# Performance work log

Measured on AMD Instinct MI355X. Metric: run time of the kernel, lower is better.

## Reference

```python
import jax, jax.numpy as jnp
import numpy as np

B, LQ, LK = 4, 256, 512
DQ = DK = PROJ = 256


def setup_inputs() -> dict:
    key = jax.random.key(0)
    ks = jax.random.split(key, 8)
    query = jax.random.normal(ks[0], (B, LQ, DQ), dtype=jnp.float32)
    keys = jax.random.normal(ks[1], (B, LK, DK), dtype=jnp.float32)
    attn_mask = jax.random.bernoulli(ks[2], 0.1, (B, LQ, LK))
    # Linear(query_size+key_size, proj) split into query/key halves (same math as concat @ W1)
    s1 = 1.0 / np.sqrt(DQ + DK)
    Wq = jax.random.uniform(ks[3], (DQ, PROJ), jnp.float32, -s1, s1)
    Wk = jax.random.uniform(ks[4], (DK, PROJ), jnp.float32, -s1, s1)
    b1 = jax.random.uniform(ks[5], (PROJ,), jnp.float32, -s1, s1)
    s2 = 1.0 / np.sqrt(PROJ)
    w2 = jax.random.uniform(ks[6], (PROJ,), jnp.float32, -s2, s2)
    b2 = jax.random.uniform(ks[7], (), jnp.float32, -s2, s2)
    return {"query": query, "keys": keys, "attn_mask": attn_mask,
            "Wq": Wq, "Wk": Wk, "b1": b1, "w2": w2, "b2": b2}


def reference(query, keys, attn_mask, Wq, Wk, b1, w2, b2):
    # cat(q_expand, k_expand) @ W1 == q@Wq broadcast-added to k@Wk (avoids the huge concat)
    qp = jnp.einsum('bqd,dp->bqp', query, Wq)            # (B,Lq,P)
    kp = jnp.einsum('bkd,dp->bkp', keys, Wk)             # (B,Lk,P)
    h = jnp.tanh(qp[:, :, None, :] + kp[:, None, :, :] + b1)  # (B,Lq,Lk,P)
    logits = jnp.einsum('bqkp,p->bqk', h, w2) + b2        # (B,Lq,Lk)
    logits = jnp.where(attn_mask, -jnp.inf, logits)
    return logits
```

## Files before the change

kernel.cpp:

```cpp
#include <hip/hip_runtime.h>
#include <math.h>

#define B_ 4
#define LQ_ 256
#define LK_ 512
#define D_ 256
#define P_ 256

#define SC 2.8853900817779268f

#define MASK_SENTINEL (-3.0e38f)


__global__ __launch_bounds__(256) void proj_kernel(
    const float* __restrict__ Q, const float* __restrict__ Kx,
    const float* __restrict__ Wq, const float* __restrict__ Wk,
    const float* __restrict__ b1,
    float* __restrict__ Eq, float* __restrict__ Ek)
{
    __shared__ __align__(16) float Ws[256][68];

    const int bm = blockIdx.x;
    const int bn = blockIdx.y;
    const bool isq = (bm < 32);
    const int m0 = isq ? bm * 32 : (bm - 32) * 32;
    const float* A = isq ? Q : Kx;
    const float* W = isq ? Wq : Wk;
    float* outp    = isq ? Eq : Ek;
    const int n0 = bn * 64;

    const int t  = threadIdx.x;
    const int tx = t & 15;
    const int ty = t >> 4;

    #pragma unroll
    for (int i = 0; i < 16; ++i) {
        int f  = t + i * 256;
        int r  = f >> 4;
        int c4 = (f & 15) * 4;
        *(float4*)&Ws[r][c4] = *(const float4*)&W[(size_t)r * P_ + n0 + c4];
    }
    __syncthreads();

    const float* arow0 = A + (size_t)(m0 + ty) * D_;
    const float* arow1 = A + (size_t)(m0 + ty + 16) * D_;

    float acc[2][4] = {};

    float4 a0c = *(const float4*)&arow0[0];
    float4 a1c = *(const float4*)&arow1[0];
    float4 w0c = *(const float4*)&Ws[0][tx * 4];
    float4 w1c = *(const float4*)&Ws[1][tx * 4];
    float4 w2c = *(const float4*)&Ws[2][tx * 4];
    float4 w3c = *(const float4*)&Ws[3][tx * 4];

    #pragma unroll 4
    for (int k4 = 0; k4 < 64; ++k4) {
        float4 a0 = a0c, a1 = a1c, w0 = w0c, w1 = w1c, w2v = w2c, w3 = w3c;
        if (k4 < 63) {
            a0c = *(const float4*)&arow0[(k4 + 1) * 4];
            a1c = *(const float4*)&arow1[(k4 + 1) * 4];
            w0c = *(const float4*)&Ws[k4 * 4 + 4][tx * 4];
            w1c = *(const float4*)&Ws[k4 * 4 + 5][tx * 4];
            w2c = *(const float4*)&Ws[k4 * 4 + 6][tx * 4];
            w3c = *(const float4*)&Ws[k4 * 4 + 7][tx * 4];
        }
        float av[2][4] = {{a0.x,a0.y,a0.z,a0.w},{a1.x,a1.y,a1.z,a1.w}};
        float wv[4][4] = {{w0.x,w0.y,w0.z,w0.w},{w1.x,w1.y,w1.z,w1.w},
                          {w2v.x,w2v.y,w2v.z,w2v.w},{w3.x,w3.y,w3.z,w3.w}};
        #pragma unroll
        for (int kk = 0; kk < 4; ++kk)
            #pragma unroll
            for (int i = 0; i < 2; ++i)
                #pragma unroll
                for (int j = 0; j < 4; ++j)
                    acc[i][j] = fmaf(av[i][kk], wv[kk][j], acc[i][j]);
    }

    float bv[4] = {0.f, 0.f, 0.f, 0.f};
    if (!isq) {
        float4 b = *(const float4*)&b1[n0 + tx * 4];
        bv[0] = b.x; bv[1] = b.y; bv[2] = b.z; bv[3] = b.w;
    }

    #pragma unroll
    for (int i = 0; i < 2; ++i) {
        int m = m0 + ty + i * 16;
        float4 o;
        o.x = __builtin_amdgcn_exp2f(SC * (acc[i][0] + bv[0]));
        o.y = __builtin_amdgcn_exp2f(SC * (acc[i][1] + bv[1]));
        o.z = __builtin_amdgcn_exp2f(SC * (acc[i][2] + bv[2]));
        o.w = __builtin_amdgcn_exp2f(SC * (acc[i][3] + bv[3]));
        *(float4*)&outp[(size_t)m * P_ + n0 + tx * 4] = o;
    }
}

__global__ __launch_bounds__(256, 4) void logits_kernel(
    const float* __restrict__ Eq, const float* __restrict__ Ek,
    const unsigned char* __restrict__ mask,
    const float* __restrict__ w2, const float* __restrict__ b2,
    float* __restrict__ out)
{
    __shared__ __align__(16) float eqs[32][132];
    __shared__ __align__(16) float eks[32][132];
    __shared__ float partial[4];

    const int b  = blockIdx.z;
    const int q0 = blockIdx.y * 32;
    const int k0 = blockIdx.x * 32;
    const int t  = threadIdx.x;

    const int tx = t & 15;
    const int ty = t >> 4;

    size_t oidx[2][2];
    unsigned char mb[2][2];
    #pragma unroll
    for (int i = 0; i < 2; ++i)
        #pragma unroll
        for (int j = 0; j < 2; ++j) {
            oidx[i][j] = (size_t)(b * LQ_ + q0 + ty + i * 16) * LK_ + (k0 + tx + j * 16);
            mb[i][j] = mask[oidx[i][j]];
        }

    float wv = w2[t];
    #pragma unroll
    for (int s = 32; s > 0; s >>= 1) wv += __shfl_xor(wv, s);
    if ((t & 63) == 0) partial[t >> 6] = wv;

    float acc[2][2] = {};

    for (int pc = 0; pc < 2; ++pc) {
        __syncthreads();
        const int p0 = pc * 128;
        #pragma unroll
        for (int i = 0; i < 2; ++i) {
            int f = t + i * 256;
            int r = f >> 5;
            int c = (f & 31) * 4;
            *(float4*)&eqs[r][c] = *(const float4*)&Eq[(size_t)(b * LQ_ + q0 + r) * P_ + p0 + c];
            *(float4*)&eks[r][c] = *(const float4*)&Ek[(size_t)(b * LK_ + k0 + r) * P_ + p0 + c];
        }
        __syncthreads();

        const float* q0p = &eqs[ty][0];
        const float* q1p = &eqs[ty + 16][0];
        const float* k0p = &eks[tx][0];
        const float* k1p = &eks[tx + 16][0];
        const float* wp  = w2 + p0;

        #pragma unroll 4
        for (int p4 = 0; p4 < 32; ++p4) {
            const float4 w = *(const float4*)&wp[p4 * 4];
            float4 qv[2], kv[2];
            qv[0] = *(const float4*)(q0p + p4 * 4);
            qv[1] = *(const float4*)(q1p + p4 * 4);
            kv[0] = *(const float4*)(k0p + p4 * 4);
            kv[1] = *(const float4*)(k1p + p4 * 4);
            float qa[2][4] = {{qv[0].x,qv[0].y,qv[0].z,qv[0].w},
                              {qv[1].x,qv[1].y,qv[1].z,qv[1].w}};
            float ka[2][4] = {{kv[0].x,kv[0].y,kv[0].z,kv[0].w},
                              {kv[1].x,kv[1].y,kv[1].z,kv[1].w}};
            #pragma unroll
            for (int i = 0; i < 2; ++i)
                #pragma unroll
                for (int j = 0; j < 2; ++j) {
                    float x0 = fmaf(qa[i][0], ka[j][0], 1.f);
                    float x1 = fmaf(qa[i][1], ka[j][1], 1.f);
                    float x2 = fmaf(qa[i][2], ka[j][2], 1.f);
                    float x3 = fmaf(qa[i][3], ka[j][3], 1.f);
                    float d01 = x0 * x1;
                    float d23 = x2 * x3;
                    float n01 = fmaf(w.x, x1, w.y * x0);
                    float n23 = fmaf(w.z, x3, w.w * x2);
                    acc[i][j] = fmaf(fmaf(n01, d23, n23 * d01),
                                     __builtin_amdgcn_rcpf(d01 * d23),
                                     acc[i][j]);
                }
        }
    }

    const float base = partial[0] + partial[1] + partial[2] + partial[3] + b2[0];

    #pragma unroll
    for (int i = 0; i < 2; ++i)
        #pragma unroll
        for (int j = 0; j < 2; ++j)
            out[oidx[i][j]] = mb[i][j] ? MASK_SENTINEL : fmaf(-2.f, acc[i][j], base);
}

extern "C" void kernel_launch(void* const* d_in, const int* in_sizes, int n_in,
                              void* d_out, int out_size, void* d_ws, size_t ws_size,
                              hipStream_t stream) {
    const float* query        = (const float*)d_in[0];
    const float* keys         = (const float*)d_in[1];
    const unsigned char* mask = (const unsigned char*)d_in[2];
    const float* Wq           = (const float*)d_in[3];
    const float* Wk           = (const float*)d_in[4];
    const float* b1           = (const float*)d_in[5];
    const float* w2           = (const float*)d_in[6];
    const float* b2           = (const float*)d_in[7];
    float* out = (float*)d_out;

    float* Eq = (float*)d_ws;
    float* Ek = Eq + (size_t)B_ * LQ_ * P_;

    dim3 g1(96, 4);
    proj_kernel<<<g1, 256, 0, stream>>>(query, keys, Wq, Wk, b1, Eq, Ek);

    dim3 g2(LK_ / 32, LQ_ / 32, B_);
    logits_kernel<<<g2, 256, 0, stream>>>(Eq, Ek, mask, w2, b2, out);
}
```

Before: 32.15 us.

## Run projection GEMM on bf16 MFMA with a prep conversion kernel

Replaces the fp32 FMA projection kernel with a bf16 MFMA kernel (16x16x32) that reads bf16 copies of the inputs and transposed weights. A new prep kernel converts query/keys to bf16 and transposes plus converts Wq/Wk each call. This is meant to cut the compute time of the projection. In exchange it adds an extra launch and extra memory traffic, and lowers precision in values that feed an exp, so error can grow.

```diff
diff --git a/kernel.cpp b/kernel.cpp
--- a/kernel.cpp
+++ b/kernel.cpp
@@ -11,87 +11,102 @@
 
 #define MASK_SENTINEL (-3.0e38f)
 
-
-__global__ __launch_bounds__(256) void proj_kernel(
+typedef __bf16 bf16x8 __attribute__((ext_vector_type(8)));
+typedef float  f32x4  __attribute__((ext_vector_type(4)));
+
+__device__ __forceinline__ unsigned short f2bf(float x) {
+    unsigned int b = __builtin_bit_cast(unsigned int, x);
+    b += 0x7FFFu + ((b >> 16) & 1u);
+    return (unsigned short)(b >> 16);
+}
+
+
+__global__ __launch_bounds__(256) void prep_kernel(
     const float* __restrict__ Q, const float* __restrict__ Kx,
     const float* __restrict__ Wq, const float* __restrict__ Wk,
+    unsigned short* __restrict__ Ab,
+    unsigned short* __restrict__ WqT, unsigned short* __restrict__ WkT)
+{
+    const int tg = blockIdx.x * 256 + threadIdx.x;
+    if (tg < 98304) {
+        const size_t i8 = (size_t)tg * 8;
+        const float* src = (i8 < (size_t)B_ * LQ_ * D_) ? (Q + i8)
+                          : (Kx + (i8 - (size_t)B_ * LQ_ * D_));
+        unsigned short o[8];
+        #pragma unroll
+        for (int j = 0; j < 8; ++j) o[j] = f2bf(src[j]);
+        *(uint4*)&Ab[i8] = *(const uint4*)o;
+    } else if (tg < 98304 + 16384) {
+        const int og  = tg - 98304;
+        const int sel = og >> 13;
+        const int o   = og & 8191;
+        const int n   = o >> 5;
+        const int k0  = (o & 31) * 8;
+        const float* W = sel ? Wk : Wq;
+        unsigned short* WT = sel ? WkT : WqT;
+        unsigned short ov[8];
+        #pragma unroll
+        for (int j = 0; j < 8; ++j) ov[j] = f2bf(W[(size_t)(k0 + j) * P_ + n]);
+        *(uint4*)&WT[(size_t)n * D_ + k0] = *(const uint4*)ov;
+    }
+}
+
+__global__ __launch_bounds__(256) void proj_mfma_kernel(
+    const unsigned short* __restrict__ Ab,
+    const unsigned short* __restrict__ WqT, const unsigned short* __restrict__ WkT,
     const float* __restrict__ b1,
     float* __restrict__ Eq, float* __restrict__ Ek)
 {
-    __shared__ __align__(16) float Ws[256][68];
-
-    const int bm = blockIdx.x;
-    const int bn = blockIdx.y;
-    const bool isq = (bm < 32);
-    const int m0 = isq ? bm * 32 : (bm - 32) * 32;
-    const float* A = isq ? Q : Kx;
-    const float* W = isq ? Wq : Wk;
-    float* outp    = isq ? Eq : Ek;
-    const int n0 = bn * 64;
-
-    const int t  = threadIdx.x;
-    const int tx = t & 15;
-    const int ty = t >> 4;
-
-    #pragma unroll
-    for (int i = 0; i < 16; ++i) {
-        int f  = t + i * 256;
-        int r  = f >> 4;
-        int c4 = (f & 15) * 4;
-        *(float4*)&Ws[r][c4] = *(const float4*)&W[(size_t)r * P_ + n0 + c4];
-    }
-    __syncthreads();
-
-    const float* arow0 = A + (size_t)(m0 + ty) * D_;
-    const float* arow1 = A + (size_t)(m0 + ty + 16) * D_;
-
-    float acc[2][4] = {};
-
-    float4 a0c = *(const float4*)&arow0[0];
-    float4 a1c = *(const float4*)&arow1[0];
-    float4 w0c = *(const float4*)&Ws[0][tx * 4];
-    float4 w1c = *(const float4*)&Ws[1][tx * 4];
-    float4 w2c = *(const float4*)&Ws[2][tx * 4];
-    float4 w3c = *(const float4*)&Ws[3][tx * 4];
-
-    #pragma unroll 4
-    for (int k4 = 0; k4 < 64; ++k4) {
-        float4 a0 = a0c, a1 = a1c, w0 = w0c, w1 = w1c, w2v = w2c, w3 = w3c;
-        if (k4 < 63) {
-            a0c = *(const float4*)&arow0[(k4 + 1) * 4];
-            a1c = *(const float4*)&arow1[(k4 + 1) * 4];
-            w0c = *(const float4*)&Ws[k4 * 4 + 4][tx * 4];
-            w1c = *(const float4*)&Ws[k4 * 4 + 5][tx * 4];
-            w2c = *(const float4*)&Ws[k4 * 4 + 6][tx * 4];
-            w3c = *(const float4*)&Ws[k4 * 4 + 7][tx * 4];
-        }
-        float av[2][4] = {{a0.x,a0.y,a0.z,a0.w},{a1.x,a1.y,a1.z,a1.w}};
-        float wv[4][4] = {{w0.x,w0.y,w0.z,w0.w},{w1.x,w1.y,w1.z,w1.w},
-                          {w2v.x,w2v.y,w2v.z,w2v.w},{w3.x,w3.y,w3.z,w3.w}};
-        #pragma unroll
-        for (int kk = 0; kk < 4; ++kk)
-            #pragma unroll
-            for (int i = 0; i < 2; ++i)
-                #pragma unroll
-                for (int j = 0; j < 4; ++j)
-                    acc[i][j] = fmaf(av[i][kk], wv[kk][j], acc[i][j]);
-    }
-
-    float bv[4] = {0.f, 0.f, 0.f, 0.f};
-    if (!isq) {
-        float4 b = *(const float4*)&b1[n0 + tx * 4];
-        bv[0] = b.x; bv[1] = b.y; bv[2] = b.z; bv[3] = b.w;
-    }
-
-    #pragma unroll
-    for (int i = 0; i < 2; ++i) {
-        int m = m0 + ty + i * 16;
-        float4 o;
-        o.x = __builtin_amdgcn_exp2f(SC * (acc[i][0] + bv[0]));
-        o.y = __builtin_amdgcn_exp2f(SC * (acc[i][1] + bv[1]));
-        o.z = __builtin_amdgcn_exp2f(SC * (acc[i][2] + bv[2]));
-        o.w = __builtin_amdgcn_exp2f(SC * (acc[i][3] + bv[3]));
-        *(float4*)&outp[(size_t)m * P_ + n0 + tx * 4] = o;
+    __shared__ __align__(16) unsigned short A_l[64][40];
+    __shared__ __align__(16) unsigned short B_l[32][40];
+
+    const int mtile = blockIdx.y;
+    const int ntile = blockIdx.x;
+    const bool isq  = (mtile < 16);
+    const int M0 = mtile * 64;
+    const int n0 = ntile * 32;
+    const unsigned short* WT = isq ? WqT : WkT;
+
+    const int t = threadIdx.x;
+    const int w = t >> 6;
+    const int l = t & 63;
+
+    f32x4 acc0 = {0.f, 0.f, 0.f, 0.f};
+    f32x4 acc1 = {0.f, 0.f, 0.f, 0.f};
+
+    for (int ks = 0; ks < 8; ++ks) {
+        __syncthreads();
+        {
+            int r = t >> 2, c = t & 3;
+            *(uint4*)&A_l[r][c * 8] =
+                *(const uint4*)&Ab[(size_t)(M0 + r) * D_ + ks * 32 + c * 8];
+        }
+        if (t < 128) {
+            int r = t >> 2, c = t & 3;
+            *(uint4*)&B_l[r][c * 8] =
+                *(const uint4*)&WT[(size_t)(n0 + r) * D_ + ks * 32 + c * 8];
+        }
+        __syncthreads();
+
+        bf16x8 af  = *(const bf16x8*)&A_l[w * 16 + (l & 15)][(l >> 4) * 8];
+        bf16x8 bf0 = *(const bf16x8*)&B_l[(l & 15)][(l >> 4) * 8];
+        bf16x8 bf1 = *(const bf16x8*)&B_l[16 + (l & 15)][(l >> 4) * 8];
+        acc0 = __builtin_amdgcn_mfma_f32_16x16x32_bf16(af, bf0, acc0, 0, 0, 0);
+        acc1 = __builtin_amdgcn_mfma_f32_16x16x32_bf16(af, bf1, acc1, 0, 0, 0);
+    }
+
+    const int col = l & 15;
+    const int rbase = (l >> 4) * 4;
+    const int mb = isq ? M0 : (M0 - 1024);
+    float* outp = isq ? Eq : Ek;
+    const float bn0 = isq ? 0.f : b1[n0 + col];
+    const float bn1 = isq ? 0.f : b1[n0 + 16 + col];
+
+    #pragma unroll
+    for (int reg = 0; reg < 4; ++reg) {
+        const int m = mb + w * 16 + rbase + reg;
+        outp[(size_t)m * P_ + n0 + col]      = __builtin_amdgcn_exp2f(SC * (acc0[reg] + bn0));
+        outp[(size_t)m * P_ + n0 + 16 + col] = __builtin_amdgcn_exp2f(SC * (acc1[reg] + bn1));
     }
 }
 
@@ -202,11 +217,17 @@
     const float* b2           = (const float*)d_in[7];
     float* out = (float*)d_out;
 
-    float* Eq = (float*)d_ws;
-    float* Ek = Eq + (size_t)B_ * LQ_ * P_;
-
-    dim3 g1(96, 4);
-    proj_kernel<<<g1, 256, 0, stream>>>(query, keys, Wq, Wk, b1, Eq, Ek);
+    char* wsb = (char*)d_ws;
+    float* Eq           = (float*)wsb;
+    float* Ek           = (float*)(wsb + 1048576);
+    unsigned short* Ab  = (unsigned short*)(wsb + 3145728);
+    unsigned short* WqT = (unsigned short*)(wsb + 4718592);
+    unsigned short* WkT = (unsigned short*)(wsb + 4849664);
+
+    prep_kernel<<<448, 256, 0, stream>>>(query, keys, Wq, Wk, Ab, WqT, WkT);
+
+    dim3 g1(8, 48);
+    proj_mfma_kernel<<<g1, 256, 0, stream>>>(Ab, WqT, WkT, b1, Eq, Ek);
 
     dim3 g2(LK_ / 32, LQ_ / 32, B_);
     logits_kernel<<<g2, 256, 0, stream>>>(Eq, Ek, mask, w2, b2, out);
```

Result: no change. 32.77 us (+1.9%).
